# Kernel optimization log

Measured on AMD Instinct MI355X. Metric: run time of the kernel, lower is better.

The kernel has to match this reference:

```python
import jax, jax.numpy as jnp
import numpy as np

B, T, X, H = 8192, 2048, 1, 4

def setup_inputs() -> dict:
    key = jax.random.key(0)
    ks = jax.random.split(key, 8)
    return {
        "x": jax.random.normal(ks[0], (B, T, X), dtype=jnp.float32),
        "y": (jax.random.uniform(ks[1], (B, T)) < 0.5).astype(jnp.float32),  # binary correctness labels
        "Wxh": jax.random.normal(ks[2], (X, H), dtype=jnp.float32) * 0.5,
        "Whh": jax.random.normal(ks[3], (H, H), dtype=jnp.float32) * 0.5,
        "bh": jax.random.normal(ks[4], (H,), dtype=jnp.float32) * 0.5,
        "Wy": jax.random.normal(ks[5], (H, 4), dtype=jnp.float32) * 0.5,
        "by": jax.random.normal(ks[6], (4,), dtype=jnp.float32) * 0.5,
        "prior": jnp.float32(0.0),
    }

def _bkt_forward(x, y, Wxh, Whh, bh, Wy, by, prior):
    # x: [B,T,X], y: [B,T]. Sequential BKT scan over time with batch vectorized.
    b = x.shape[0]
    h0 = jnp.zeros((b, Wy.shape[0]), dtype=x.dtype)
    lat0 = jnp.full((b,), prior, dtype=x.dtype)

    def step(carry, xt):
        h, latent = carry
        p = jax.nn.sigmoid(h @ Wy + by)          # [B,4] -> (learn l, forget f, guess g, slip s)
        l, f, g, s = p[:, 0], p[:, 1], p[:, 2], p[:, 3]
        correct = latent * (1 - s) + (1 - latent) * g
        k_t1 = latent * (1 - s) / correct
        k_t0 = latent * s / (latent * s + (1 - latent) * (1 - g))
        m_t = k_t1 * correct + k_t0 * (1 - correct)
        new_latent = m_t * (1 - f) + (1 - m_t) * l
        h_new = jax.nn.sigmoid(xt @ Wxh + h @ Whh + bh)  # [B,H]
        return (h_new, new_latent), (correct, new_latent)

    xs = jnp.swapaxes(x, 0, 1)                   # [T,B,X]
    _, (corrects, latents) = jax.lax.scan(step, (h0, lat0), xs)
    corrects = jnp.swapaxes(corrects, 0, 1)      # [B,T]
    latents = jnp.swapaxes(latents, 0, 1)        # [B,T]
    eps = jnp.float32(1e-7)
    c = jnp.clip(corrects, eps, 1 - eps)
    loss = -jnp.mean(y * jnp.log(c) + (1 - y) * jnp.log1p(-c))
    return corrects, latents, loss

def reference(x, y, Wxh, Whh, bh, Wy, by, prior):
    return _bkt_forward(x, y, Wxh, Whh, bh, Wy, by, prior)
```

## Files before the change

kernel.cpp:

```cpp
#include <hip/hip_runtime.h>

#define BB 8192
#define TT 2048
#define CLW 16
#define WU  8

typedef __fp16 f16x2 __attribute__((ext_vector_type(2)));

__device__ __forceinline__ float sig2(float z) {
    return __builtin_amdgcn_rcpf(1.f + __builtin_amdgcn_exp2f(z));
}
__device__ __forceinline__ float sgpr(float v) {
    return __builtin_bit_cast(float, __builtin_amdgcn_readfirstlane(__builtin_bit_cast(int, v)));
}
__device__ __forceinline__ void ld16(float* d, const float* p) {
    *(float4*)(d)      = *(const float4*)(p);
    *(float4*)(d + 4)  = *(const float4*)(p + 4);
    *(float4*)(d + 8)  = *(const float4*)(p + 8);
    *(float4*)(d + 12) = *(const float4*)(p + 12);
}

__global__ __launch_bounds__(256, 5) void bkt_fused(
    const float* __restrict__ x, const float* __restrict__ y,
    const float* __restrict__ Wxh, const float* __restrict__ Whh,
    const float* __restrict__ bh, const float* __restrict__ Wy,
    const float* __restrict__ by, const float* __restrict__ prior,
    float* __restrict__ corrects, float* __restrict__ latents,
    float* __restrict__ partials)
{
    __shared__ float lds[4 * 2 * 32 * 33];
    __shared__ float2 hand[2];
    const int tid  = blockIdx.x * 256 + threadIdx.x;
    const int lane = threadIdx.x & 63;
    const int wv   = threadIdx.x >> 6;
    const int half = wv & 1;
    const int rib  = wv >> 1;
    const int row  = blockIdx.x * 2 + rib;
    float* r0 = &lds[wv * 2112];
    float* r1 = r0 + 1056;
    const int wbase = (lane >> 1) * 33 + (lane & 1) * 16;
    const float NL2E = -1.44269504088896340736f;

    const float wh00=sgpr(Whh[0]*NL2E),  wh01=sgpr(Whh[1]*NL2E),
                wh02=sgpr(Whh[2]*NL2E),  wh03=sgpr(Whh[3]*NL2E),
                wh10=sgpr(Whh[4]*NL2E),  wh11=sgpr(Whh[5]*NL2E),
                wh12=sgpr(Whh[6]*NL2E),  wh13=sgpr(Whh[7]*NL2E),
                wh20=sgpr(Whh[8]*NL2E),  wh21=sgpr(Whh[9]*NL2E),
                wh22=sgpr(Whh[10]*NL2E), wh23=sgpr(Whh[11]*NL2E),
                wh30=sgpr(Whh[12]*NL2E), wh31=sgpr(Whh[13]*NL2E),
                wh32=sgpr(Whh[14]*NL2E), wh33=sgpr(Whh[15]*NL2E);
    const float wx0=sgpr(Wxh[0]*NL2E), wx1=sgpr(Wxh[1]*NL2E),
                wx2=sgpr(Wxh[2]*NL2E), wx3=sgpr(Wxh[3]*NL2E);
    const float bh0=sgpr(bh[0]*NL2E), bh1=sgpr(bh[1]*NL2E),
                bh2=sgpr(bh[2]*NL2E), bh3=sgpr(bh[3]*NL2E);
    const float wy00=sgpr(Wy[0]*NL2E),  wy01=sgpr(Wy[1]*NL2E),
                wy02=sgpr(Wy[2]*NL2E),  wy03=sgpr(Wy[3]*NL2E),
                wy10=sgpr(Wy[4]*NL2E),  wy11=sgpr(Wy[5]*NL2E),
                wy12=sgpr(Wy[6]*NL2E),  wy13=sgpr(Wy[7]*NL2E),
                wy20=sgpr(Wy[8]*NL2E),  wy21=sgpr(Wy[9]*NL2E),
                wy22=sgpr(Wy[10]*NL2E), wy23=sgpr(Wy[11]*NL2E),
                wy30=sgpr(Wy[12]*NL2E), wy31=sgpr(Wy[13]*NL2E),
                wy32=sgpr(Wy[14]*NL2E), wy33=sgpr(Wy[15]*NL2E);
    const float by0=sgpr(by[0]*NL2E), by1=sgpr(by[1]*NL2E),
                by2=sgpr(by[2]*NL2E), by3=sgpr(by[3]*NL2E);
    const float pr = sgpr(prior[0]);

#define HSTEP(xs)                                                                   \
    {                                                                               \
        float z0 = fmaf(h3,wh30,fmaf(h2,wh20,fmaf(h1,wh10,fmaf(h0,wh00,fmaf(xs,wx0,bh0))))); \
        float z1 = fmaf(h3,wh31,fmaf(h2,wh21,fmaf(h1,wh11,fmaf(h0,wh01,fmaf(xs,wx1,bh1))))); \
        float z2 = fmaf(h3,wh32,fmaf(h2,wh22,fmaf(h1,wh12,fmaf(h0,wh02,fmaf(xs,wx2,bh2))))); \
        float z3 = fmaf(h3,wh33,fmaf(h2,wh23,fmaf(h1,wh13,fmaf(h0,wh03,fmaf(xs,wx3,bh3))))); \
        h0 = sig2(z0); h1 = sig2(z1); h2 = sig2(z2); h3 = sig2(z3);                 \
    }

    const int c  = half * 64 + lane;
    const int t0 = c * CLW;
    const float* xrow = x + (size_t)row * TT;
    float* crow = corrects + (size_t)row * TT + half * 1024;
    float* lrow = latents  + (size_t)row * TT + half * 1024;

    float xw[8], xb[16];
    {
        const float* wp = xrow + (c ? t0 - WU : 0);
        *(float4*)(xw)     = *(const float4*)(wp);
        *(float4*)(xw + 4) = *(const float4*)(wp + 4);
    }
    ld16(xb, xrow + t0);

    float h0 = 0.f, h1 = 0.f, h2 = 0.f, h3 = 0.f;
    HSTEP(xw[0])  HSTEP(xw[1])  HSTEP(xw[2])  HSTEP(xw[3])
    HSTEP(xw[4])  HSTEP(xw[5])  HSTEP(xw[6])  HSTEP(xw[7])
    if (c == 0) { h0 = h1 = h2 = h3 = 0.f; }

    float Aacc = 1.f, Bacc = 0.f;
#define S1(s, DO_H)                                                                 \
    {                                                                               \
        float zl = fmaf(h3,wy30,fmaf(h2,wy20,fmaf(h1,wy10,fmaf(h0,wy00,by0))));     \
        float zf = fmaf(h3,wy31,fmaf(h2,wy21,fmaf(h1,wy11,fmaf(h0,wy01,by1))));     \
        float zg = fmaf(h3,wy32,fmaf(h2,wy22,fmaf(h1,wy12,fmaf(h0,wy02,by2))));     \
        float zs = fmaf(h3,wy33,fmaf(h2,wy23,fmaf(h1,wy13,fmaf(h0,wy03,by3))));     \
        float pl = sig2(zl), pf = sig2(zf), pgs = sig2(zg), pss = sig2(zs);         \
        float a = (1.f - pf) - pl;                                                  \
        Bacc = fmaf(a, Bacc, pl);                                                   \
        Aacc *= a;                                                                  \
        f16x2 pk0 = __builtin_amdgcn_cvt_pkrtz(pgs, (1.f - pss) - pgs);             \
        f16x2 pk1 = __builtin_amdgcn_cvt_pkrtz(Aacc, Bacc);                         \
        r0[wbase + (s)] = __builtin_bit_cast(float, pk0);                           \
        r1[wbase + (s)] = __builtin_bit_cast(float, pk1);                           \
        DO_H                                                                        \
    }
    S1(0,  HSTEP(xb[0]))  S1(1,  HSTEP(xb[1]))  S1(2,  HSTEP(xb[2]))
    S1(3,  HSTEP(xb[3]))  S1(4,  HSTEP(xb[4]))  S1(5,  HSTEP(xb[5]))
    S1(6,  HSTEP(xb[6]))  S1(7,  HSTEP(xb[7]))  S1(8,  HSTEP(xb[8]))
    S1(9,  HSTEP(xb[9]))  S1(10, HSTEP(xb[10])) S1(11, HSTEP(xb[11]))
    S1(12, HSTEP(xb[12])) S1(13, HSTEP(xb[13])) S1(14, HSTEP(xb[14]))
    S1(15, )
#undef S1

    float yb[16];
    ld16(yb, y + (size_t)row * TT + t0);

    float As = Aacc, Bs = Bacc;
#pragma unroll
    for (int off = 1; off < 64; off <<= 1) {
        float Au = __shfl_up(As, off);
        float Bu = __shfl_up(Bs, off);
        if (lane >= off) { Bs = fmaf(As, Bu, Bs); As *= Au; }
    }
    if (half == 0 && lane == 63) hand[rib] = make_float2(As, Bs);
    __syncthreads();
    float pr_base = pr;
    if (half) { const float2 hv = hand[rib]; pr_base = fmaf(hv.x, pr, hv.y); }
    const float Ae = __shfl_up(As, 1);
    const float Be = __shfl_up(Bs, 1);
    const float lat0 = (lane == 0) ? pr_base : fmaf(Ae, pr_base, Be);

    float lacc = 0.f, prod = 1.f, latp = lat0;
#define E(s)                                                                        \
    {                                                                               \
        f16x2 pk0 = __builtin_bit_cast(f16x2, r0[wbase + (s)]);                     \
        f16x2 pk1 = __builtin_bit_cast(f16x2, r1[wbase + (s)]);                     \
        float cv = fmaf(latp, (float)pk0[1], (float)pk0[0]);                        \
        latp = fmaf((float)pk1[0], lat0, (float)pk1[1]);                            \
        float cc  = fminf(fmaxf(cv, 1e-7f), 1.f - 1e-7f);                           \
        prod *= fmaf(yb[s], fmaf(2.f, cc, -1.f), 1.f - cc);                         \
        r0[wbase + (s)] = cv;                                                       \
    }
    E(0) E(1) E(2) E(3) E(4) E(5) E(6) E(7)
    lacc += __builtin_amdgcn_logf(prod); prod = 1.f;
    E(8) E(9) E(10) E(11) E(12) E(13) E(14) E(15)
    lacc += __builtin_amdgcn_logf(prod);
#undef E

#pragma unroll
    for (int j = 0; j < 4; ++j) {
        const int base = (8 * j + (lane >> 3)) * 33 + 4 * (lane & 7);
        float4 v = make_float4(r0[base], r0[base + 1], r0[base + 2], r0[base + 3]);
        *(float4*)(crow + j * 256 + 4 * lane) = v;
    }
#pragma unroll
    for (int s = 0; s < 16; ++s) {
        f16x2 pk1 = __builtin_bit_cast(f16x2, r1[wbase + s]);
        r1[wbase + s] = fmaf((float)pk1[0], lat0, (float)pk1[1]);
    }
#pragma unroll
    for (int j = 0; j < 4; ++j) {
        const int base = (8 * j + (lane >> 3)) * 33 + 4 * (lane & 7);
        float4 v = make_float4(r1[base], r1[base + 1], r1[base + 2], r1[base + 3]);
        *(float4*)(lrow + j * 256 + 4 * lane) = v;
    }

#pragma unroll
    for (int off = 32; off; off >>= 1) lacc += __shfl_down(lacc, off);
    if (lane == 0) partials[tid >> 6] = lacc;
#undef HSTEP
}

__global__ __launch_bounds__(1024) void bkt_loss(const float* __restrict__ partials, int n,
                                                 float* __restrict__ out_loss)
{
    __shared__ double sd[16];
    double s = 0.0;
    for (int i = threadIdx.x; i < n; i += 1024) s += (double)partials[i];
#pragma unroll
    for (int off = 32; off; off >>= 1) s += __shfl_down(s, off);
    if ((threadIdx.x & 63) == 0) sd[threadIdx.x >> 6] = s;
    __syncthreads();
    if (threadIdx.x == 0) {
        double t = 0.0;
#pragma unroll
        for (int k = 0; k < 16; ++k) t += sd[k];
        *out_loss = (float)(-t * 0.69314718055994530942 / ((double)BB * (double)TT));
    }
}

extern "C" void kernel_launch(void* const* d_in, const int* in_sizes, int n_in,
                              void* d_out, int out_size, void* d_ws, size_t ws_size,
                              hipStream_t stream)
{
    const float* x     = (const float*)d_in[0];
    const float* y     = (const float*)d_in[1];
    const float* Wxh   = (const float*)d_in[2];
    const float* Whh   = (const float*)d_in[3];
    const float* bh    = (const float*)d_in[4];
    const float* Wy    = (const float*)d_in[5];
    const float* by    = (const float*)d_in[6];
    const float* prior = (const float*)d_in[7];

    float* out      = (float*)d_out;
    float* corrects = out;
    float* latents  = out + (size_t)BB * TT;
    float* lossp    = out + (size_t)2 * BB * TT;

    float* partials = (float*)d_ws;

    const int nblk = BB / 2;
    bkt_fused<<<nblk, 256, 0, stream>>>(x, y, Wxh, Whh, bh, Wy, by, prior,
                                        corrects, latents, partials);
    bkt_loss<<<1, 1024, 0, stream>>>(partials, BB * 2, lossp);
}
```

Before: 66.44 us.

## Map one wave per row with 32-step chunks and register-held latent coefficients

```diff
diff --git a/kernel.cpp b/kernel.cpp
--- a/kernel.cpp
+++ b/kernel.cpp
@@ -2,7 +2,6 @@
 
 #define BB 8192
 #define TT 2048
-#define CLW 16
 #define WU  8
 
 typedef __fp16 f16x2 __attribute__((ext_vector_type(2)));
@@ -20,7 +19,7 @@
     *(float4*)(d + 12) = *(const float4*)(p + 12);
 }
 
-__global__ __launch_bounds__(256, 5) void bkt_fused(
+__global__ __launch_bounds__(256, 3) void bkt_fused(
     const float* __restrict__ x, const float* __restrict__ y,
     const float* __restrict__ Wxh, const float* __restrict__ Whh,
     const float* __restrict__ bh, const float* __restrict__ Wy,
@@ -28,17 +27,13 @@
     float* __restrict__ corrects, float* __restrict__ latents,
     float* __restrict__ partials)
 {
-    __shared__ float lds[4 * 2 * 32 * 33];
-    __shared__ float2 hand[2];
+    __shared__ float lds[4 * 64 * 33];
     const int tid  = blockIdx.x * 256 + threadIdx.x;
     const int lane = threadIdx.x & 63;
     const int wv   = threadIdx.x >> 6;
-    const int half = wv & 1;
-    const int rib  = wv >> 1;
-    const int row  = blockIdx.x * 2 + rib;
+    const int row  = blockIdx.x * 4 + wv;
     float* r0 = &lds[wv * 2112];
-    float* r1 = r0 + 1056;
-    const int wbase = (lane >> 1) * 33 + (lane & 1) * 16;
+    const int wbase = lane * 33;
     const float NL2E = -1.44269504088896340736f;
 
     const float wh00=sgpr(Whh[0]*NL2E),  wh01=sgpr(Whh[1]*NL2E),
@@ -74,27 +69,30 @@
         h0 = sig2(z0); h1 = sig2(z1); h2 = sig2(z2); h3 = sig2(z3);                 \
     }
 
-    const int c  = half * 64 + lane;
-    const int t0 = c * CLW;
+    const int t0 = lane * 32;
     const float* xrow = x + (size_t)row * TT;
-    float* crow = corrects + (size_t)row * TT + half * 1024;
-    float* lrow = latents  + (size_t)row * TT + half * 1024;
-
-    float xw[8], xb[16];
+    const float* yrow = y + (size_t)row * TT;
+    float* crow = corrects + (size_t)row * TT;
+    float* lrow = latents  + (size_t)row * TT;
+
+    float xw[8], xb[16], xc[16];
     {
-        const float* wp = xrow + (c ? t0 - WU : 0);
+        const float* wp = xrow + (lane ? t0 - WU : 0);
         *(float4*)(xw)     = *(const float4*)(wp);
         *(float4*)(xw + 4) = *(const float4*)(wp + 4);
     }
     ld16(xb, xrow + t0);
+    ld16(xc, xrow + t0 + 16);
 
     float h0 = 0.f, h1 = 0.f, h2 = 0.f, h3 = 0.f;
     HSTEP(xw[0])  HSTEP(xw[1])  HSTEP(xw[2])  HSTEP(xw[3])
     HSTEP(xw[4])  HSTEP(xw[5])  HSTEP(xw[6])  HSTEP(xw[7])
-    if (c == 0) { h0 = h1 = h2 = h3 = 0.f; }
-
+    if (lane == 0) { h0 = h1 = h2 = h3 = 0.f; }
+
+    float apl[32];
+    float Ack[7], Bck[7];
     float Aacc = 1.f, Bacc = 0.f;
-#define S1(s, DO_H)                                                                 \
+#define S1(s, DO_H, DO_CK)                                                          \
     {                                                                               \
         float zl = fmaf(h3,wy30,fmaf(h2,wy20,fmaf(h1,wy10,fmaf(h0,wy00,by0))));     \
         float zf = fmaf(h3,wy31,fmaf(h2,wy21,fmaf(h1,wy11,fmaf(h0,wy01,by1))));     \
@@ -105,21 +103,31 @@
         Bacc = fmaf(a, Bacc, pl);                                                   \
         Aacc *= a;                                                                  \
         f16x2 pk0 = __builtin_amdgcn_cvt_pkrtz(pgs, (1.f - pss) - pgs);             \
-        f16x2 pk1 = __builtin_amdgcn_cvt_pkrtz(Aacc, Bacc);                         \
+        f16x2 pk1 = __builtin_amdgcn_cvt_pkrtz(a, pl);                              \
         r0[wbase + (s)] = __builtin_bit_cast(float, pk0);                           \
-        r1[wbase + (s)] = __builtin_bit_cast(float, pk1);                           \
+        apl[s] = __builtin_bit_cast(float, pk1);                                    \
+        DO_CK                                                                       \
         DO_H                                                                        \
     }
-    S1(0,  HSTEP(xb[0]))  S1(1,  HSTEP(xb[1]))  S1(2,  HSTEP(xb[2]))
-    S1(3,  HSTEP(xb[3]))  S1(4,  HSTEP(xb[4]))  S1(5,  HSTEP(xb[5]))
-    S1(6,  HSTEP(xb[6]))  S1(7,  HSTEP(xb[7]))  S1(8,  HSTEP(xb[8]))
-    S1(9,  HSTEP(xb[9]))  S1(10, HSTEP(xb[10])) S1(11, HSTEP(xb[11]))
-    S1(12, HSTEP(xb[12])) S1(13, HSTEP(xb[13])) S1(14, HSTEP(xb[14]))
-    S1(15, )
+#define CK(k) Ack[k] = Aacc; Bck[k] = Bacc;
+    S1(0,  HSTEP(xb[0]),  )  S1(1,  HSTEP(xb[1]),  )
+    S1(2,  HSTEP(xb[2]),  )  S1(3,  HSTEP(xb[3]),  CK(0))
+    S1(4,  HSTEP(xb[4]),  )  S1(5,  HSTEP(xb[5]),  )
+    S1(6,  HSTEP(xb[6]),  )  S1(7,  HSTEP(xb[7]),  CK(1))
+    S1(8,  HSTEP(xb[8]),  )  S1(9,  HSTEP(xb[9]),  )
+    S1(10, HSTEP(xb[10]), )  S1(11, HSTEP(xb[11]), CK(2))
+    S1(12, HSTEP(xb[12]), )  S1(13, HSTEP(xb[13]), )
+    S1(14, HSTEP(xb[14]), )  S1(15, HSTEP(xb[15]), CK(3))
+    S1(16, HSTEP(xc[0]),  )  S1(17, HSTEP(xc[1]),  )
+    S1(18, HSTEP(xc[2]),  )  S1(19, HSTEP(xc[3]),  CK(4))
+    S1(20, HSTEP(xc[4]),  )  S1(21, HSTEP(xc[5]),  )
+    S1(22, HSTEP(xc[6]),  )  S1(23, HSTEP(xc[7]),  CK(5))
+    S1(24, HSTEP(xc[8]),  )  S1(25, HSTEP(xc[9]),  )
+    S1(26, HSTEP(xc[10]), )  S1(27, HSTEP(xc[11]), CK(6))
+    S1(28, HSTEP(xc[12]), )  S1(29, HSTEP(xc[13]), )
+    S1(30, HSTEP(xc[14]), )  S1(31, , )
+#undef CK
 #undef S1
-
-    float yb[16];
-    ld16(yb, y + (size_t)row * TT + t0);
 
     float As = Aacc, Bs = Bacc;
 #pragma unroll
@@ -128,47 +136,70 @@
         float Bu = __shfl_up(Bs, off);
         if (lane >= off) { Bs = fmaf(As, Bu, Bs); As *= Au; }
     }
-    if (half == 0 && lane == 63) hand[rib] = make_float2(As, Bs);
-    __syncthreads();
-    float pr_base = pr;
-    if (half) { const float2 hv = hand[rib]; pr_base = fmaf(hv.x, pr, hv.y); }
     const float Ae = __shfl_up(As, 1);
     const float Be = __shfl_up(Bs, 1);
-    const float lat0 = (lane == 0) ? pr_base : fmaf(Ae, pr_base, Be);
-
+    const float lat0 = (lane == 0) ? pr : fmaf(Ae, pr, Be);
+
+    float yb[16];
+    ld16(yb, yrow + t0);
     float lacc = 0.f, prod = 1.f, latp = lat0;
-#define E(s)                                                                        \
+#define E(s, Y)                                                                     \
     {                                                                               \
         f16x2 pk0 = __builtin_bit_cast(f16x2, r0[wbase + (s)]);                     \
-        f16x2 pk1 = __builtin_bit_cast(f16x2, r1[wbase + (s)]);                     \
+        f16x2 pk1 = __builtin_bit_cast(f16x2, apl[s]);                              \
         float cv = fmaf(latp, (float)pk0[1], (float)pk0[0]);                        \
-        latp = fmaf((float)pk1[0], lat0, (float)pk1[1]);                            \
+        latp = fmaf((float)pk1[0], latp, (float)pk1[1]);                            \
         float cc  = fminf(fmaxf(cv, 1e-7f), 1.f - 1e-7f);                           \
-        prod *= fmaf(yb[s], fmaf(2.f, cc, -1.f), 1.f - cc);                         \
+        prod *= fmaf(Y[(s) & 15], fmaf(2.f, cc, -1.f), 1.f - cc);                   \
         r0[wbase + (s)] = cv;                                                       \
     }
-    E(0) E(1) E(2) E(3) E(4) E(5) E(6) E(7)
+#define RST(k) latp = fmaf(Ack[k], lat0, Bck[k]);
+    E(0, yb)  E(1, yb)  E(2, yb)  E(3, yb)  RST(0)
+    E(4, yb)  E(5, yb)  E(6, yb)  E(7, yb)  RST(1)
     lacc += __builtin_amdgcn_logf(prod); prod = 1.f;
-    E(8) E(9) E(10) E(11) E(12) E(13) E(14) E(15)
+    E(8, yb)  E(9, yb)  E(10, yb) E(11, yb) RST(2)
+    E(12, yb) E(13, yb) E(14, yb) E(15, yb) RST(3)
+    lacc += __builtin_amdgcn_logf(prod); prod = 1.f;
+    ld16(yb, yrow + t0 + 16);
+    E(16, yb) E(17, yb) E(18, yb) E(19, yb) RST(4)
+    E(20, yb) E(21, yb) E(22, yb) E(23, yb) RST(5)
+    lacc += __builtin_amdgcn_logf(prod); prod = 1.f;
+    E(24, yb) E(25, yb) E(26, yb) E(27, yb) RST(6)
+    E(28, yb) E(29, yb) E(30, yb) E(31, yb)
     lacc += __builtin_amdgcn_logf(prod);
 #undef E
-
-#pragma unroll
-    for (int j = 0; j < 4; ++j) {
-        const int base = (8 * j + (lane >> 3)) * 33 + 4 * (lane & 7);
+#undef RST
+
+#pragma unroll
+    for (int k = 0; k < 8; ++k) {
+        const int base = (8 * k + (lane >> 3)) * 33 + 4 * (lane & 7);
         float4 v = make_float4(r0[base], r0[base + 1], r0[base + 2], r0[base + 3]);
-        *(float4*)(crow + j * 256 + 4 * lane) = v;
-    }
-#pragma unroll
-    for (int s = 0; s < 16; ++s) {
-        f16x2 pk1 = __builtin_bit_cast(f16x2, r1[wbase + s]);
-        r1[wbase + s] = fmaf((float)pk1[0], lat0, (float)pk1[1]);
-    }
-#pragma unroll
-    for (int j = 0; j < 4; ++j) {
-        const int base = (8 * j + (lane >> 3)) * 33 + 4 * (lane & 7);
-        float4 v = make_float4(r1[base], r1[base + 1], r1[base + 2], r1[base + 3]);
-        *(float4*)(lrow + j * 256 + 4 * lane) = v;
+        *(float4*)(crow + k * 256 + 4 * lane) = v;
+    }
+    {
+        float latq = lat0;
+#pragma unroll
+        for (int s = 0; s < 4; ++s) {
+            f16x2 pk1 = __builtin_bit_cast(f16x2, apl[s]);
+            latq = fmaf((float)pk1[0], latq, (float)pk1[1]);
+            r0[wbase + s] = latq;
+        }
+#define L4(s0, KPREV)                                                               \
+        { latq = fmaf(Ack[KPREV], lat0, Bck[KPREV]);                                \
+          _Pragma("unroll")                                                         \
+          for (int s = (s0); s < (s0) + 4; ++s) {                                   \
+              f16x2 pk1 = __builtin_bit_cast(f16x2, apl[s]);                        \
+              latq = fmaf((float)pk1[0], latq, (float)pk1[1]);                      \
+              r0[wbase + s] = latq;                                                 \
+          } }
+        L4(4, 0) L4(8, 1) L4(12, 2) L4(16, 3) L4(20, 4) L4(24, 5) L4(28, 6)
+#undef L4
+    }
+#pragma unroll
+    for (int k = 0; k < 8; ++k) {
+        const int base = (8 * k + (lane >> 3)) * 33 + 4 * (lane & 7);
+        float4 v = make_float4(r0[base], r0[base + 1], r0[base + 2], r0[base + 3]);
+        *(float4*)(lrow + k * 256 + 4 * lane) = v;
     }
 
 #pragma unroll
@@ -215,8 +246,8 @@
 
     float* partials = (float*)d_ws;
 
-    const int nblk = BB / 2;
+    const int nblk = BB / 4;
     bkt_fused<<<nblk, 256, 0, stream>>>(x, y, Wxh, Whh, bh, Wy, by, prior,
                                         corrects, latents, partials);
-    bkt_loss<<<1, 1024, 0, stream>>>(partials, BB * 2, lossp);
-}
+    bkt_loss<<<1, 1024, 0, stream>>>(partials, BB, lossp);
+}
```

Measured after the change: 63.29 us, median of 2. 4.7% less time.
